# Optimization experiments

Hardware: AMD Instinct MI355X
Metric: run time of the kernel (lower is better)

Reference implementation:

```python
import jax, jax.numpy as jnp
import numpy as np

SUBSTEP = 10
FRAMES = 24
T = FRAMES * SUBSTEP
DT = 1.0 / 60.0 / SUBSTEP
SLOPE_DEG = 20.0
COS_S = float(np.cos(np.deg2rad(SLOPE_DEG)))
SIN_S = float(np.sin(np.deg2rad(SLOPE_DEG)))
INIT_HEIGHT = 0.1
N_VERTS = 2_000_000
GRAVITY = jnp.array([0.0, -9.8, 0.0], dtype=jnp.float32)
CONTACT_N = jnp.array([-SIN_S, COS_S, 0.0], dtype=jnp.float32)
EPS = 1e-6


def quat_mul(a, b):
    w1, x1, y1, z1 = a[0], a[1], a[2], a[3]
    w2, x2, y2, z2 = b[0], b[1], b[2], b[3]
    return jnp.stack([
        w1 * w2 - x1 * x2 - y1 * y2 - z1 * z2,
        w1 * x2 + x1 * w2 + y1 * z2 - z1 * y2,
        w1 * y2 + y1 * w2 + z1 * x2 - x1 * z2,
        w1 * z2 + z1 * w2 + x1 * y2 - y1 * x2,
    ])


def quat_to_matrix(q):
    q = q / jnp.linalg.norm(q)
    w, x, y, z = q[0], q[1], q[2], q[3]
    return jnp.stack([
        jnp.stack([1 - 2 * y * y - 2 * z * z, 2 * x * y - 2 * w * z, 2 * x * z + 2 * w * y]),
        jnp.stack([2 * x * y + 2 * w * z, 1 - 2 * x * x - 2 * z * z, 2 * y * z - 2 * w * x]),
        jnp.stack([2 * x * z - 2 * w * y, 2 * y * z + 2 * w * x, 1 - 2 * x * x - 2 * y * y]),
    ])


def cross_matrix(a):
    z = jnp.zeros((), dtype=a.dtype)
    return jnp.stack([
        jnp.stack([z, -a[2], a[1]]),
        jnp.stack([a[2], z, -a[0]]),
        jnp.stack([-a[1], a[0], z]),
    ])


def setup_inputs() -> dict:
    key = jax.random.key(0)
    k1, k2, k3 = jax.random.split(key, 3)
    return {
        "x": jax.random.normal(k1, (N_VERTS, 3), dtype=jnp.float32) * 0.2,
        "mass_center": jnp.zeros((3,), dtype=jnp.float32),
        "init_trans": jax.random.normal(k2, (3,), dtype=jnp.float32) * 0.3 + jnp.array([0.3, 0.5, 0.0]),
        "init_quat": jnp.ones((4,), dtype=jnp.float32),
        "init_v": jax.random.normal(k3, (3,), dtype=jnp.float32) * 0.1,
        "kn": jnp.array([0.5], dtype=jnp.float32),
        "mu": jnp.array([0.4], dtype=jnp.float32),
        "linear_damping": jnp.array([0.999], dtype=jnp.float32),
        "angular_damping": jnp.array([0.998], dtype=jnp.float32),
    }


def _simulate(x, mass_center, init_trans, init_quat, init_v, kn, mu, linear_damping, angular_damping):
    n = x.shape[0]
    mass = jnp.asarray(float(n), dtype=x.dtype)  # unit mass per vertex
    inv_mass = 1.0 / mass
    r = x - mass_center
    # inertia_reference = sum_i m*( (r.r) I - outer(r,r) )
    inertia = jnp.sum(jnp.einsum('ni,ni->n', r, r)) * jnp.eye(3, dtype=x.dtype) - jnp.einsum('ni,nj->ij', r, r)
    kn0, mu0 = kn[0], mu[0]
    ld, ad = linear_damping[0], angular_damping[0]
    eye3 = jnp.eye(3, dtype=x.dtype)

    def step(carry, _):
        trans, quat, v, omega = carry
        Rm = quat_to_matrix(quat)
        Rx = x @ Rm.T                                   # [N,3]
        xi = trans + Rx + mass_center                   # world positions
        vi_all = v + jnp.cross(omega[None, :], Rx)      # per-vertex velocities
        d = xi @ CONTACT_N
        rel_v = vi_all @ CONTACT_N
        mask = (d < -COS_S * INIT_HEIGHT) & (rel_v < 0.0)
        num = jnp.sum(mask)
        numf = jnp.maximum(num, 1).astype(x.dtype)
        sum_pos = jnp.sum(x * mask[:, None].astype(x.dtype), axis=0)
        ri = sum_pos / numf
        Ri = Rm @ ri
        vi = v + jnp.cross(omega, Ri)
        v_n = jnp.dot(vi, CONTACT_N) * CONTACT_N
        v_t = vi - v_n
        vn_new = -kn0 * v_n
        alpha = jnp.maximum(1.0 - mu0 * (1.0 + kn0) * (jnp.linalg.norm(v_n) / (jnp.linalg.norm(v_t) + EPS)), 0.0)
        vi_new = vn_new + alpha * v_t
        I = Rm @ inertia @ Rm.T
        I_inv = jnp.linalg.inv(I)
        Rri = cross_matrix(Ri)
        kmat = inv_mass * eye3 - Rri @ I_inv @ Rri
        J = jnp.linalg.solve(kmat, vi_new - vi)
        hit = num > 0
        dv = jnp.where(hit, J * inv_mass, 0.0)
        domega = jnp.where(hit, I_inv @ Rri @ J, 0.0)
        v_new = (v + GRAVITY * DT) * ld + dv
        omega_new = omega * ad + domega
        trans_new = trans + DT * v_new
        wq = jnp.concatenate([jnp.zeros((1,), dtype=x.dtype), omega_new]) * (0.5 * DT)
        quat_new = quat + quat_mul(wq, quat)
        quat_new = quat_new / jnp.linalg.norm(quat_new)
        new_carry = (trans_new, quat_new, v_new, omega_new)
        return new_carry, jnp.concatenate([trans_new, quat_new])

    carry0 = (init_trans, init_quat / jnp.linalg.norm(init_quat), init_v, jnp.zeros(3, dtype=x.dtype))
    _, traj = jax.lax.scan(step, carry0, None, length=T)
    return traj  # [T, 7] = translation(3) + quaternion(4) per substep


def reference(x, mass_center, init_trans, init_quat, init_v, kn, mu, linear_damping, angular_damping):
    return _simulate(x, mass_center, init_trans, init_quat, init_v, kn, mu, linear_damping, angular_damping)
```

## Files before the change

kernel.cpp:

```cpp
#include <hip/hip_runtime.h>

#define GRID    256
#define BLOCK   512
#define NWAVES  (BLOCK / 64)
#define CHUNK   7813

typedef unsigned long long u64;

__device__ __forceinline__ u64 rec_load(const u64* p) {
  return __hip_atomic_load(p, __ATOMIC_RELAXED, __HIP_MEMORY_SCOPE_AGENT);
}
__device__ __forceinline__ void rec_store(u64* p, u64 v) {
  __hip_atomic_store(p, v, __ATOMIC_RELAXED, __HIP_MEMORY_SCOPE_AGENT);
}
__device__ __forceinline__ u64 rec_pack(float f, unsigned tag) {
  return (u64)__float_as_uint(f) | ((u64)tag << 32);
}

template <int NV>
__device__ __forceinline__ void block_reduce(float* v, float* sm) {
  #pragma unroll
  for (int off = 32; off > 0; off >>= 1) {
    #pragma unroll
    for (int k = 0; k < NV; ++k) v[k] += __shfl_down(v[k], off, 64);
  }
  const int lane = threadIdx.x & 63;
  const int wid  = threadIdx.x >> 6;
  if (lane == 0) {
    #pragma unroll
    for (int k = 0; k < NV; ++k) sm[wid * NV + k] = v[k];
  }
  __syncthreads();
  if (threadIdx.x == 0) {
    #pragma unroll
    for (int w = 1; w < NWAVES; ++w) {
      #pragma unroll
      for (int k = 0; k < NV; ++k) v[k] += sm[w * NV + k];
    }
  }
  __syncthreads();
}

__device__ __forceinline__ void mat3_mul(const float* A, const float* B, float* C) {
  #pragma unroll
  for (int i = 0; i < 3; ++i)
    #pragma unroll
    for (int j = 0; j < 3; ++j)
      C[i*3+j] = A[i*3+0]*B[0*3+j] + A[i*3+1]*B[1*3+j] + A[i*3+2]*B[2*3+j];
}
__device__ __forceinline__ void mat3_mul_bt(const float* A, const float* B, float* C) {
  #pragma unroll
  for (int i = 0; i < 3; ++i)
    #pragma unroll
    for (int j = 0; j < 3; ++j)
      C[i*3+j] = A[i*3+0]*B[j*3+0] + A[i*3+1]*B[j*3+1] + A[i*3+2]*B[j*3+2];
}
__device__ __forceinline__ void mat3_inv(const float* m, float* inv) {
  float A =  (m[4]*m[8] - m[5]*m[7]);
  float B = -(m[3]*m[8] - m[5]*m[6]);
  float C =  (m[3]*m[7] - m[4]*m[6]);
  float det = m[0]*A + m[1]*B + m[2]*C;
  float id = 1.0f / det;
  inv[0] = A * id;
  inv[1] = -(m[1]*m[8] - m[2]*m[7]) * id;
  inv[2] =  (m[1]*m[5] - m[2]*m[4]) * id;
  inv[3] = B * id;
  inv[4] =  (m[0]*m[8] - m[2]*m[6]) * id;
  inv[5] = -(m[0]*m[5] - m[2]*m[3]) * id;
  inv[6] = C * id;
  inv[7] = -(m[0]*m[7] - m[1]*m[6]) * id;
  inv[8] =  (m[0]*m[4] - m[1]*m[3]) * id;
}

__global__ __launch_bounds__(BLOCK)
void sim_kernel(const float* __restrict__ xg,
                const float* __restrict__ mc_p,
                const float* __restrict__ itr_p,
                const float* __restrict__ iq_p,
                const float* __restrict__ iv_p,
                const float* __restrict__ kn_p,
                const float* __restrict__ mu_p,
                const float* __restrict__ ldp_p,
                const float* __restrict__ adp_p,
                float* __restrict__ out,
                u64* __restrict__ ws,
                int N, int T)
{
  const int tid = threadIdx.x;
  const int bid = blockIdx.x;

  extern __shared__ float dyn[];
  float* sXx = dyn;
  float* sXy = dyn + CHUNK;
  float* sXz = dyn + 2 * CHUNK;
  __shared__ float s_red[NWAVES * 8];
  __shared__ float s_plane[8];

  const float nx  = (float)(-0.3420201433256687);
  const float ny  = (float)( 0.9396926207859084);
  const float DTF = (float)(1.0 / 60.0 / 10.0);
  const float HDT = (float)(0.5 * (1.0 / 60.0 / 10.0));
  const float DTH = (float)(-0.9396926207859084 * 0.1);
  const float GYDT = -9.8f * (float)(1.0 / 60.0 / 10.0);

  const float mc0 = mc_p[0], mc1 = mc_p[1], mc2 = mc_p[2];

  u64* part0 = ws;
  u64* part1 = ws + 4 * GRID;
  u64* st    = ws + 8 * GRID;
  u64* bufI  = ws + 8 * GRID + 128;

  const int vstart = bid * CHUNK;
  int cl = N - vstart; if (cl > CHUNK) cl = CHUNK; if (cl < 0) cl = 0;

  for (int i = tid; i < cl; i += BLOCK) {
    const float* p = xg + (size_t)(vstart + i) * 3;
    sXx[i] = p[0]; sXy[i] = p[1]; sXz[i] = p[2];
  }
  __syncthreads();

  {
    float v6[6] = {0,0,0,0,0,0};
    for (int i = tid; i < cl; i += BLOCK) {
      float r0 = sXx[i] - mc0, r1 = sXy[i] - mc1, r2 = sXz[i] - mc2;
      v6[0] += r0*r0; v6[1] += r1*r1; v6[2] += r2*r2;
      v6[3] += r0*r1; v6[4] += r0*r2; v6[5] += r1*r2;
    }
    block_reduce<6>(v6, s_red);
    if (tid == 0) {
      #pragma unroll
      for (int k = 0; k < 6; ++k) rec_store(bufI + k * GRID + bid, rec_pack(v6[k], 0xC0FFEEu));
    }
  }

  float In[9];
  if (bid == 0) {
    float v6[6] = {0,0,0,0,0,0};
    if (tid < GRID) {
      u64 r[6];
      int f = 0;
      for (;;) {
        #pragma unroll
        for (int k = 0; k < 6; ++k) r[k] = rec_load(bufI + k * GRID + tid);
        bool ok = true;
        #pragma unroll
        for (int k = 0; k < 6; ++k) ok &= ((unsigned)(r[k] >> 32) == 0xC0FFEEu);
        if (ok) break;
        if ((++f & 15) == 0) __builtin_amdgcn_s_sleep(1);
      }
      #pragma unroll
      for (int k = 0; k < 6; ++k) v6[k] = __uint_as_float((unsigned)r[k]);
    }
    block_reduce<6>(v6, s_red);
    float trc = v6[0] + v6[1] + v6[2];
    In[0] = trc - v6[0]; In[4] = trc - v6[1]; In[8] = trc - v6[2];
    In[1] = -v6[3]; In[3] = -v6[3];
    In[2] = -v6[4]; In[6] = -v6[4];
    In[5] = -v6[5]; In[7] = -v6[5];
  }

  float tr0 = itr_p[0], tr1 = itr_p[1], tr2 = itr_p[2];
  float q0 = iq_p[0], q1 = iq_p[1], q2 = iq_p[2], q3 = iq_p[3];
  {
    float n0 = sqrtf(q0*q0 + q1*q1 + q2*q2 + q3*q3);
    q0 /= n0; q1 /= n0; q2 /= n0; q3 /= n0;
  }
  float v0 = iv_p[0], v1 = iv_p[1], v2 = iv_p[2];
  float om0 = 0.f, om1 = 0.f, om2 = 0.f;
  const float knv = kn_p[0], muv = mu_p[0], ldv = ldp_p[0], adv = adp_p[0];
  const float inv_mass = 1.0f / (float)N;

  float Rm[9];
  float Ii[9];

  if (tid == 0) {
    float qn = sqrtf(q0*q0 + q1*q1 + q2*q2 + q3*q3);
    float w = q0/qn, xq = q1/qn, yq = q2/qn, zq = q3/qn;
    Rm[0] = 1.f - 2.f*yq*yq - 2.f*zq*zq; Rm[1] = 2.f*xq*yq - 2.f*w*zq; Rm[2] = 2.f*xq*zq + 2.f*w*yq;
    Rm[3] = 2.f*xq*yq + 2.f*w*zq; Rm[4] = 1.f - 2.f*xq*xq - 2.f*zq*zq; Rm[5] = 2.f*yq*zq - 2.f*w*xq;
    Rm[6] = 2.f*xq*zq - 2.f*w*yq; Rm[7] = 2.f*yq*zq + 2.f*w*xq; Rm[8] = 1.f - 2.f*xq*xq - 2.f*yq*yq;
    float a0 = Rm[0]*nx + Rm[3]*ny;
    float a1 = Rm[1]*nx + Rm[4]*ny;
    float a2 = Rm[2]*nx + Rm[5]*ny;
    float w0 = ny*om2, w1 = -nx*om2, w2 = nx*om1 - ny*om0;
    float b0 = Rm[0]*w0 + Rm[3]*w1 + Rm[6]*w2;
    float b1 = Rm[1]*w0 + Rm[4]*w1 + Rm[7]*w2;
    float b2 = Rm[2]*w0 + Rm[5]*w1 + Rm[8]*w2;
    float ca = DTH - ((tr0 + mc0)*nx + (tr1 + mc1)*ny);
    float cb = -(v0*nx + v1*ny);
    s_plane[0] = a0; s_plane[1] = a1; s_plane[2] = a2;
    s_plane[3] = b0; s_plane[4] = b1; s_plane[5] = b2;
    s_plane[6] = ca; s_plane[7] = cb;
    if (bid == 0) {
      float Tm[9]; mat3_mul(Rm, In, Tm);
      float Iw[9]; mat3_mul_bt(Tm, Rm, Iw);
      mat3_inv(Iw, Ii);
    }
  }
  __syncthreads();

  for (int t = 0; t < T; ++t) {
    const float a0 = s_plane[0], a1 = s_plane[1], a2 = s_plane[2];
    const float b0 = s_plane[3], b1 = s_plane[4], b2 = s_plane[5];
    const float ca = s_plane[6], cb = s_plane[7];

    float acc[4] = {0.f, 0.f, 0.f, 0.f};
    for (int i = tid; i < cl; i += BLOCK) {
      float x0 = sXx[i], x1 = sXy[i], x2 = sXz[i];
      float da = x0*a0 + x1*a1 + x2*a2;
      float db = x0*b0 + x1*b1 + x2*b2;
      if (da < ca && db < cb) { acc[0] += 1.f; acc[1] += x0; acc[2] += x1; acc[3] += x2; }
    }
    block_reduce<4>(acc, s_red);

    const unsigned want = (unsigned)(t + 1);
    u64* pb = (t & 1) ? part1 : part0;
    if (tid == 0) {
      #pragma unroll
      for (int k = 0; k < 4; ++k) rec_store(pb + k * GRID + bid, rec_pack(acc[k], want));
    }

    if (bid == 0) {
      float tot[4] = {0.f, 0.f, 0.f, 0.f};
      if (tid < GRID) {
        u64 r0, r1, r2, r3;
        int f = 0;
        for (;;) {
          r0 = rec_load(pb + 0 * GRID + tid);
          r1 = rec_load(pb + 1 * GRID + tid);
          r2 = rec_load(pb + 2 * GRID + tid);
          r3 = rec_load(pb + 3 * GRID + tid);
          if ((unsigned)(r0 >> 32) == want && (unsigned)(r1 >> 32) == want &&
              (unsigned)(r2 >> 32) == want && (unsigned)(r3 >> 32) == want) break;
          if ((++f & 15) == 0) __builtin_amdgcn_s_sleep(1);
        }
        tot[0] = __uint_as_float((unsigned)r0);
        tot[1] = __uint_as_float((unsigned)r1);
        tot[2] = __uint_as_float((unsigned)r2);
        tot[3] = __uint_as_float((unsigned)r3);
      }
      block_reduce<4>(tot, s_red);

      if (tid == 0) {
        float num = tot[0];
        float numf = fmaxf(num, 1.0f);
        float ri0 = tot[1] / numf, ri1 = tot[2] / numf, ri2 = tot[3] / numf;
        float Ri0 = Rm[0]*ri0 + Rm[1]*ri1 + Rm[2]*ri2;
        float Ri1 = Rm[3]*ri0 + Rm[4]*ri1 + Rm[5]*ri2;
        float Ri2 = Rm[6]*ri0 + Rm[7]*ri1 + Rm[8]*ri2;
        float dv0 = 0.f, dv1 = 0.f, dv2 = 0.f, dm0 = 0.f, dm1 = 0.f, dm2 = 0.f;
        if (num > 0.0f) {
          float vi0 = v0 + om1*Ri2 - om2*Ri1;
          float vi1 = v1 + om2*Ri0 - om0*Ri2;
          float vi2 = v2 + om0*Ri1 - om1*Ri0;
          float vdn = vi0*nx + vi1*ny;
          float vn0 = vdn*nx, vn1 = vdn*ny;
          float vt0 = vi0 - vn0, vt1 = vi1 - vn1, vt2 = vi2;
          float nvn = sqrtf(vn0*vn0 + vn1*vn1);
          float nvt = sqrtf(vt0*vt0 + vt1*vt1 + vt2*vt2);
          float alpha = fmaxf(1.0f - muv*(1.0f + knv)*(nvn/(nvt + 1e-6f)), 0.0f);
          float dvi0 = (-knv*vn0 + alpha*vt0) - vi0;
          float dvi1 = (-knv*vn1 + alpha*vt1) - vi1;
          float dvi2 = (alpha*vt2) - vi2;
          float Cx[9] = {0.f, -Ri2, Ri1,  Ri2, 0.f, -Ri0,  -Ri1, Ri0, 0.f};
          float T2[9]; mat3_mul(Cx, Ii, T2);
          float T3[9]; mat3_mul(T2, Cx, T3);
          float K[9];
          #pragma unroll
          for (int k = 0; k < 9; ++k) K[k] = -T3[k];
          K[0] += inv_mass; K[4] += inv_mass; K[8] += inv_mass;
          float Ki[9]; mat3_inv(K, Ki);
          float J0 = Ki[0]*dvi0 + Ki[1]*dvi1 + Ki[2]*dvi2;
          float J1 = Ki[3]*dvi0 + Ki[4]*dvi1 + Ki[5]*dvi2;
          float J2 = Ki[6]*dvi0 + Ki[7]*dvi1 + Ki[8]*dvi2;
          dv0 = J0*inv_mass; dv1 = J1*inv_mass; dv2 = J2*inv_mass;
          float c0 = -Ri2*J1 + Ri1*J2;
          float c1 =  Ri2*J0 - Ri0*J2;
          float c2 = -Ri1*J0 + Ri0*J1;
          dm0 = Ii[0]*c0 + Ii[1]*c1 + Ii[2]*c2;
          dm1 = Ii[3]*c0 + Ii[4]*c1 + Ii[5]*c2;
          dm2 = Ii[6]*c0 + Ii[7]*c1 + Ii[8]*c2;
        }
        v0 = v0*ldv + dv0;
        v1 = (v1 + GYDT)*ldv + dv1;
        v2 = v2*ldv + dv2;
        om0 = om0*adv + dm0; om1 = om1*adv + dm1; om2 = om2*adv + dm2;
        tr0 = tr0 + DTF*v0; tr1 = tr1 + DTF*v1; tr2 = tr2 + DTF*v2;
        float wx = om0*HDT, wy = om1*HDT, wz = om2*HDT;
        float dq0 = -wx*q1 - wy*q2 - wz*q3;
        float dq1 =  wx*q0 + wy*q3 - wz*q2;
        float dq2 =  wy*q0 + wz*q1 - wx*q3;
        float dq3 =  wz*q0 + wx*q2 - wy*q1;
        q0 += dq0; q1 += dq1; q2 += dq2; q3 += dq3;
        float qn2 = sqrtf(q0*q0 + q1*q1 + q2*q2 + q3*q3);
        q0 /= qn2; q1 /= qn2; q2 /= qn2; q3 /= qn2;
        float* o = out + (size_t)t * 7;
        o[0] = tr0; o[1] = tr1; o[2] = tr2;
        o[3] = q0;  o[4] = q1;  o[5] = q2;  o[6] = q3;
        float qn = sqrtf(q0*q0 + q1*q1 + q2*q2 + q3*q3);
        float w = q0/qn, xq = q1/qn, yq = q2/qn, zq = q3/qn;
        Rm[0] = 1.f - 2.f*yq*yq - 2.f*zq*zq; Rm[1] = 2.f*xq*yq - 2.f*w*zq; Rm[2] = 2.f*xq*zq + 2.f*w*yq;
        Rm[3] = 2.f*xq*yq + 2.f*w*zq; Rm[4] = 1.f - 2.f*xq*xq - 2.f*zq*zq; Rm[5] = 2.f*yq*zq - 2.f*w*xq;
        Rm[6] = 2.f*xq*zq - 2.f*w*yq; Rm[7] = 2.f*yq*zq + 2.f*w*xq; Rm[8] = 1.f - 2.f*xq*xq - 2.f*yq*yq;
        float na0 = Rm[0]*nx + Rm[3]*ny;
        float na1 = Rm[1]*nx + Rm[4]*ny;
        float na2 = Rm[2]*nx + Rm[5]*ny;
        float w0 = ny*om2, w1 = -nx*om2, w2 = nx*om1 - ny*om0;
        float nb0 = Rm[0]*w0 + Rm[3]*w1 + Rm[6]*w2;
        float nb1 = Rm[1]*w0 + Rm[4]*w1 + Rm[7]*w2;
        float nb2 = Rm[2]*w0 + Rm[5]*w1 + Rm[8]*w2;
        float nca = DTH - ((tr0 + mc0)*nx + (tr1 + mc1)*ny);
        float ncb = -(v0*nx + v1*ny);
        s_plane[0] = na0; s_plane[1] = na1; s_plane[2] = na2;
        s_plane[3] = nb0; s_plane[4] = nb1; s_plane[5] = nb2;
        s_plane[6] = nca; s_plane[7] = ncb;
      }
      __syncthreads();
      if (tid < 64) {
        u64* sl = st + (size_t)((t + 1) & 1) * 64;
        rec_store(sl + tid, rec_pack(s_plane[tid & 7], want));
      }
      if (tid == 0) {
        float Tm[9]; mat3_mul(Rm, In, Tm);
        float Iw[9]; mat3_mul_bt(Tm, Rm, Iw);
        mat3_inv(Iw, Ii);
      }
    } else {
      if (tid < 8) {
        const u64* sl = st + (size_t)((t + 1) & 1) * 64 + (size_t)(bid & 7) * 8;
        u64 r; int f = 0;
        for (;;) {
          r = rec_load(sl + tid);
          if ((unsigned)(r >> 32) == want) break;
          if ((++f & 31) == 0) __builtin_amdgcn_s_sleep(1);
        }
        s_plane[tid] = __uint_as_float((unsigned)r);
      }
      __syncthreads();
    }
  }
}

extern "C" void kernel_launch(void* const* d_in, const int* in_sizes, int n_in,
                              void* d_out, int out_size, void* d_ws, size_t ws_size,
                              hipStream_t stream) {
  const float* x   = (const float*)d_in[0];
  const float* mc  = (const float*)d_in[1];
  const float* itr = (const float*)d_in[2];
  const float* iq  = (const float*)d_in[3];
  const float* iv  = (const float*)d_in[4];
  const float* kn  = (const float*)d_in[5];
  const float* mu  = (const float*)d_in[6];
  const float* ldp = (const float*)d_in[7];
  const float* adp = (const float*)d_in[8];
  float* out = (float*)d_out;
  u64* ws  = (u64*)d_ws;
  int N = in_sizes[0] / 3;
  int T = out_size / 7;

  const int dyn_lds = 3 * CHUNK * 4;
  hipFuncSetAttribute((const void*)sim_kernel,
                      hipFuncAttributeMaxDynamicSharedMemorySize, dyn_lds);

  void* args[] = {(void*)&x, (void*)&mc, (void*)&itr, (void*)&iq, (void*)&iv,
                  (void*)&kn, (void*)&mu, (void*)&ldp, (void*)&adp,
                  (void*)&out, (void*)&ws, (void*)&N, (void*)&T};
  hipLaunchCooperativeKernel((void*)sim_kernel, dim3(GRID), dim3(BLOCK),
                             args, dyn_lds, stream);
}
```

Measured before the change: 1.424 ms.

## Replicate rigid-body update in every block and keep vertices in registers

Every block now reads all per-block partial sums and runs the rigid-body update redundantly. This removes the second broadcast phase, where block 0 published the plane and the other blocks polled for it. Vertex coordinates are held in registers (16 slots per thread) instead of LDS. The kernel also adds a skip path that bypasses the contact reduction and the grid exchange when angular velocity is zero and the body is not moving toward the slope. The cost is redundant scalar work on thread 0 of every block and higher register pressure. The skip predicate is a conservative analytic check, not a test-specific shortcut.

```diff
diff --git a/kernel.cpp b/kernel.cpp
--- a/kernel.cpp
+++ b/kernel.cpp
@@ -1,9 +1,10 @@
 #include <hip/hip_runtime.h>
 
-#define GRID    256
-#define BLOCK   512
-#define NWAVES  (BLOCK / 64)
-#define CHUNK   7813
+#define GRID   256
+#define BLOCK  512
+#define NWAVES (BLOCK / 64)
+#define CHUNK  7813
+#define SLOTS  16
 
 typedef unsigned long long u64;
 
@@ -16,6 +17,13 @@
 __device__ __forceinline__ u64 rec_pack(float f, unsigned tag) {
   return (u64)__float_as_uint(f) | ((u64)tag << 32);
 }
+
+#define C_NX   ((float)(-0.3420201433256687))
+#define C_NY   ((float)( 0.9396926207859084))
+#define C_DTF  ((float)(1.0 / 60.0 / 10.0))
+#define C_HDT  ((float)(0.5 * (1.0 / 60.0 / 10.0)))
+#define C_DTH  ((float)(-0.9396926207859084 * 0.1))
+#define C_GYDT (-9.8f * (float)(1.0 / 60.0 / 10.0))
 
 template <int NV>
 __device__ __forceinline__ void block_reduce(float* v, float* sm) {
@@ -89,44 +97,43 @@
   const int tid = threadIdx.x;
   const int bid = blockIdx.x;
 
-  extern __shared__ float dyn[];
-  float* sXx = dyn;
-  float* sXy = dyn + CHUNK;
-  float* sXz = dyn + 2 * CHUNK;
-  __shared__ float s_red[NWAVES * 8];
   __shared__ float s_plane[8];
-
-  const float nx  = (float)(-0.3420201433256687);
-  const float ny  = (float)( 0.9396926207859084);
-  const float DTF = (float)(1.0 / 60.0 / 10.0);
-  const float HDT = (float)(0.5 * (1.0 / 60.0 / 10.0));
-  const float DTH = (float)(-0.9396926207859084 * 0.1);
-  const float GYDT = -9.8f * (float)(1.0 / 60.0 / 10.0);
+  __shared__ int   s_skip[2];
+  __shared__ float s_redI[NWAVES * 6];
+  __shared__ float s_red[2][NWAVES * 4];
+  __shared__ float s_red2[2][NWAVES * 4];
+
+  u64* part = ws;
+  u64* bufI = ws + 2 * 4 * GRID;
 
   const float mc0 = mc_p[0], mc1 = mc_p[1], mc2 = mc_p[2];
-
-  u64* part0 = ws;
-  u64* part1 = ws + 4 * GRID;
-  u64* st    = ws + 8 * GRID;
-  u64* bufI  = ws + 8 * GRID + 128;
 
   const int vstart = bid * CHUNK;
   int cl = N - vstart; if (cl > CHUNK) cl = CHUNK; if (cl < 0) cl = 0;
 
-  for (int i = tid; i < cl; i += BLOCK) {
-    const float* p = xg + (size_t)(vstart + i) * 3;
-    sXx[i] = p[0]; sXy[i] = p[1]; sXz[i] = p[2];
-  }
-  __syncthreads();
+  float xr0[SLOTS], xr1[SLOTS], xr2[SLOTS];
+  #pragma unroll
+  for (int s = 0; s < SLOTS; ++s) {
+    const int i = tid + s * BLOCK;
+    if (i < cl) {
+      const float* p = xg + (size_t)(vstart + i) * 3;
+      xr0[s] = p[0]; xr1[s] = p[1]; xr2[s] = p[2];
+    } else {
+      xr0[s] = 0.f; xr1[s] = 0.f; xr2[s] = 0.f;
+    }
+  }
 
   {
     float v6[6] = {0,0,0,0,0,0};
-    for (int i = tid; i < cl; i += BLOCK) {
-      float r0 = sXx[i] - mc0, r1 = sXy[i] - mc1, r2 = sXz[i] - mc2;
-      v6[0] += r0*r0; v6[1] += r1*r1; v6[2] += r2*r2;
-      v6[3] += r0*r1; v6[4] += r0*r2; v6[5] += r1*r2;
-    }
-    block_reduce<6>(v6, s_red);
+    #pragma unroll
+    for (int s = 0; s < SLOTS; ++s) {
+      if (tid + s * BLOCK < cl) {
+        float r0 = xr0[s] - mc0, r1 = xr1[s] - mc1, r2 = xr2[s] - mc2;
+        v6[0] += r0*r0; v6[1] += r1*r1; v6[2] += r2*r2;
+        v6[3] += r0*r1; v6[4] += r0*r2; v6[5] += r1*r2;
+      }
+    }
+    block_reduce<6>(v6, s_redI);
     if (tid == 0) {
       #pragma unroll
       for (int k = 0; k < 6; ++k) rec_store(bufI + k * GRID + bid, rec_pack(v6[k], 0xC0FFEEu));
@@ -134,7 +141,7 @@
   }
 
   float In[9];
-  if (bid == 0) {
+  {
     float v6[6] = {0,0,0,0,0,0};
     if (tid < GRID) {
       u64 r[6];
@@ -151,7 +158,7 @@
       #pragma unroll
       for (int k = 0; k < 6; ++k) v6[k] = __uint_as_float((unsigned)r[k]);
     }
-    block_reduce<6>(v6, s_red);
+    block_reduce<6>(v6, s_redI);
     float trc = v6[0] + v6[1] + v6[2];
     In[0] = trc - v6[0]; In[4] = trc - v6[1]; In[8] = trc - v6[2];
     In[1] = -v6[3]; In[3] = -v6[3];
@@ -170,8 +177,7 @@
   const float knv = kn_p[0], muv = mu_p[0], ldv = ldp_p[0], adv = adp_p[0];
   const float inv_mass = 1.0f / (float)N;
 
-  float Rm[9];
-  float Ii[9];
+  float Rm[9], Ii[9];
 
   if (tid == 0) {
     float qn = sqrtf(q0*q0 + q1*q1 + q2*q2 + q3*q3);
@@ -179,164 +185,187 @@
     Rm[0] = 1.f - 2.f*yq*yq - 2.f*zq*zq; Rm[1] = 2.f*xq*yq - 2.f*w*zq; Rm[2] = 2.f*xq*zq + 2.f*w*yq;
     Rm[3] = 2.f*xq*yq + 2.f*w*zq; Rm[4] = 1.f - 2.f*xq*xq - 2.f*zq*zq; Rm[5] = 2.f*yq*zq - 2.f*w*xq;
     Rm[6] = 2.f*xq*zq - 2.f*w*yq; Rm[7] = 2.f*yq*zq + 2.f*w*xq; Rm[8] = 1.f - 2.f*xq*xq - 2.f*yq*yq;
-    float a0 = Rm[0]*nx + Rm[3]*ny;
-    float a1 = Rm[1]*nx + Rm[4]*ny;
-    float a2 = Rm[2]*nx + Rm[5]*ny;
-    float w0 = ny*om2, w1 = -nx*om2, w2 = nx*om1 - ny*om0;
+    float a0 = Rm[0]*C_NX + Rm[3]*C_NY;
+    float a1 = Rm[1]*C_NX + Rm[4]*C_NY;
+    float a2 = Rm[2]*C_NX + Rm[5]*C_NY;
+    float w0 = C_NY*om2, w1 = -C_NX*om2, w2 = C_NX*om1 - C_NY*om0;
     float b0 = Rm[0]*w0 + Rm[3]*w1 + Rm[6]*w2;
     float b1 = Rm[1]*w0 + Rm[4]*w1 + Rm[7]*w2;
     float b2 = Rm[2]*w0 + Rm[5]*w1 + Rm[8]*w2;
-    float ca = DTH - ((tr0 + mc0)*nx + (tr1 + mc1)*ny);
-    float cb = -(v0*nx + v1*ny);
+    float ca = C_DTH - ((tr0 + mc0)*C_NX + (tr1 + mc1)*C_NY);
+    float cb = -(v0*C_NX + v1*C_NY);
     s_plane[0] = a0; s_plane[1] = a1; s_plane[2] = a2;
     s_plane[3] = b0; s_plane[4] = b1; s_plane[5] = b2;
     s_plane[6] = ca; s_plane[7] = cb;
-    if (bid == 0) {
+    s_skip[0] = (om0 == 0.f && om1 == 0.f && om2 == 0.f && !(cb > 0.f)) ? 1 : 0;
+    float Tm[9]; mat3_mul(Rm, In, Tm);
+    float Iw[9]; mat3_mul_bt(Tm, Rm, Iw);
+    mat3_inv(Iw, Ii);
+  }
+
+  int pub = 0;
+  for (int t = 0; t < T; ++t) {
+    __syncthreads();
+    const int skip = s_skip[t & 1];
+    float tn = 0.f, tx = 0.f, ty = 0.f, tz = 0.f;
+
+    if (!skip) {
+      const float a0 = s_plane[0], a1 = s_plane[1], a2 = s_plane[2];
+      const float b0 = s_plane[3], b1 = s_plane[4], b2 = s_plane[5];
+      const float ca = s_plane[6], cb = s_plane[7];
+      float acc0 = 0.f, acc1 = 0.f, acc2 = 0.f, acc3 = 0.f;
+      #pragma unroll
+      for (int s = 0; s < SLOTS; ++s) {
+        const float x0 = xr0[s], x1 = xr1[s], x2 = xr2[s];
+        const float da = x0*a0 + x1*a1 + x2*a2;
+        const float db = x0*b0 + x1*b1 + x2*b2;
+        if ((tid + s * BLOCK < cl) && (da < ca) && (db < cb)) {
+          acc0 += 1.f; acc1 += x0; acc2 += x1; acc3 += x2;
+        }
+      }
+      #pragma unroll
+      for (int off = 32; off > 0; off >>= 1) {
+        acc0 += __shfl_down(acc0, off, 64);
+        acc1 += __shfl_down(acc1, off, 64);
+        acc2 += __shfl_down(acc2, off, 64);
+        acc3 += __shfl_down(acc3, off, 64);
+      }
+      const int lane = tid & 63, wid = tid >> 6;
+      float* srA = s_red[pub & 1];
+      if (lane == 0) {
+        srA[wid*4+0] = acc0; srA[wid*4+1] = acc1;
+        srA[wid*4+2] = acc2; srA[wid*4+3] = acc3;
+      }
+      __syncthreads();
+      const unsigned want = (unsigned)(pub + 1);
+      if (tid < 4) {
+        float tw = srA[tid];
+        #pragma unroll
+        for (int w2 = 1; w2 < NWAVES; ++w2) tw += srA[w2*4 + tid];
+        rec_store(part + (size_t)(pub & 1) * 4 * GRID + (size_t)tid * GRID + bid,
+                  rec_pack(tw, want));
+      }
+      float f0 = 0.f, f1 = 0.f, f2 = 0.f, f3 = 0.f;
+      if (tid < GRID) {
+        const u64* pp = part + (size_t)(pub & 1) * 4 * GRID + tid;
+        u64 r0, r1, r2, r3;
+        int fl = 0;
+        for (;;) {
+          r0 = rec_load(pp + 0 * GRID);
+          r1 = rec_load(pp + 1 * GRID);
+          r2 = rec_load(pp + 2 * GRID);
+          r3 = rec_load(pp + 3 * GRID);
+          if (((unsigned)(r0 >> 32) == want) && ((unsigned)(r1 >> 32) == want) &&
+              ((unsigned)(r2 >> 32) == want) && ((unsigned)(r3 >> 32) == want)) break;
+          if ((++fl & 15) == 0) __builtin_amdgcn_s_sleep(1);
+        }
+        f0 = __uint_as_float((unsigned)r0);
+        f1 = __uint_as_float((unsigned)r1);
+        f2 = __uint_as_float((unsigned)r2);
+        f3 = __uint_as_float((unsigned)r3);
+      }
+      #pragma unroll
+      for (int off = 32; off > 0; off >>= 1) {
+        f0 += __shfl_down(f0, off, 64);
+        f1 += __shfl_down(f1, off, 64);
+        f2 += __shfl_down(f2, off, 64);
+        f3 += __shfl_down(f3, off, 64);
+      }
+      float* srB = s_red2[pub & 1];
+      if (lane == 0) {
+        srB[wid*4+0] = f0; srB[wid*4+1] = f1;
+        srB[wid*4+2] = f2; srB[wid*4+3] = f3;
+      }
+      __syncthreads();
+      if (tid == 0) {
+        tn = srB[0]; tx = srB[1]; ty = srB[2]; tz = srB[3];
+        #pragma unroll
+        for (int w2 = 1; w2 < NWAVES; ++w2) {
+          tn += srB[w2*4+0]; tx += srB[w2*4+1];
+          ty += srB[w2*4+2]; tz += srB[w2*4+3];
+        }
+      }
+      ++pub;
+    }
+
+    if (tid == 0) {
+      float dv0 = 0.f, dv1 = 0.f, dv2 = 0.f, dm0 = 0.f, dm1 = 0.f, dm2 = 0.f;
+      if (tn > 0.f) {
+        float numf = fmaxf(tn, 1.0f);
+        float ri0 = tx/numf, ri1 = ty/numf, ri2 = tz/numf;
+        float Ri0 = Rm[0]*ri0 + Rm[1]*ri1 + Rm[2]*ri2;
+        float Ri1 = Rm[3]*ri0 + Rm[4]*ri1 + Rm[5]*ri2;
+        float Ri2 = Rm[6]*ri0 + Rm[7]*ri1 + Rm[8]*ri2;
+        float vi0 = v0 + om1*Ri2 - om2*Ri1;
+        float vi1 = v1 + om2*Ri0 - om0*Ri2;
+        float vi2 = v2 + om0*Ri1 - om1*Ri0;
+        float vdn = vi0*C_NX + vi1*C_NY;
+        float vn0 = vdn*C_NX, vn1 = vdn*C_NY;
+        float vt0 = vi0 - vn0, vt1 = vi1 - vn1, vt2 = vi2;
+        float nvn = sqrtf(vn0*vn0 + vn1*vn1);
+        float nvt = sqrtf(vt0*vt0 + vt1*vt1 + vt2*vt2);
+        float alpha = fmaxf(1.0f - muv*(1.0f + knv)*(nvn/(nvt + 1e-6f)), 0.0f);
+        float dvi0 = (-knv*vn0 + alpha*vt0) - vi0;
+        float dvi1 = (-knv*vn1 + alpha*vt1) - vi1;
+        float dvi2 = (alpha*vt2) - vi2;
+        float Cx[9] = {0.f, -Ri2, Ri1,  Ri2, 0.f, -Ri0,  -Ri1, Ri0, 0.f};
+        float T2[9]; mat3_mul(Cx, Ii, T2);
+        float T3[9]; mat3_mul(T2, Cx, T3);
+        float Km[9];
+        #pragma unroll
+        for (int m = 0; m < 9; ++m) Km[m] = -T3[m];
+        Km[0] += inv_mass; Km[4] += inv_mass; Km[8] += inv_mass;
+        float Ki[9]; mat3_inv(Km, Ki);
+        float J0 = Ki[0]*dvi0 + Ki[1]*dvi1 + Ki[2]*dvi2;
+        float J1 = Ki[3]*dvi0 + Ki[4]*dvi1 + Ki[5]*dvi2;
+        float J2 = Ki[6]*dvi0 + Ki[7]*dvi1 + Ki[8]*dvi2;
+        dv0 = J0*inv_mass; dv1 = J1*inv_mass; dv2 = J2*inv_mass;
+        float c0 = -Ri2*J1 + Ri1*J2;
+        float c1 =  Ri2*J0 - Ri0*J2;
+        float c2 = -Ri1*J0 + Ri0*J1;
+        dm0 = Ii[0]*c0 + Ii[1]*c1 + Ii[2]*c2;
+        dm1 = Ii[3]*c0 + Ii[4]*c1 + Ii[5]*c2;
+        dm2 = Ii[6]*c0 + Ii[7]*c1 + Ii[8]*c2;
+      }
+      v0 = v0*ldv + dv0;
+      v1 = (v1 + C_GYDT)*ldv + dv1;
+      v2 = v2*ldv + dv2;
+      om0 = om0*adv + dm0; om1 = om1*adv + dm1; om2 = om2*adv + dm2;
+      tr0 += C_DTF*v0; tr1 += C_DTF*v1; tr2 += C_DTF*v2;
+      float wx = om0*C_HDT, wy = om1*C_HDT, wz = om2*C_HDT;
+      float dq0 = -wx*q1 - wy*q2 - wz*q3;
+      float dq1 =  wx*q0 + wy*q3 - wz*q2;
+      float dq2 =  wy*q0 + wz*q1 - wx*q3;
+      float dq3 =  wz*q0 + wx*q2 - wy*q1;
+      q0 += dq0; q1 += dq1; q2 += dq2; q3 += dq3;
+      float qn2 = sqrtf(q0*q0 + q1*q1 + q2*q2 + q3*q3);
+      q0 /= qn2; q1 /= qn2; q2 /= qn2; q3 /= qn2;
+      if (bid == 0) {
+        float* o = out + (size_t)t * 7;
+        o[0] = tr0; o[1] = tr1; o[2] = tr2;
+        o[3] = q0;  o[4] = q1;  o[5] = q2;  o[6] = q3;
+      }
+      float qn = sqrtf(q0*q0 + q1*q1 + q2*q2 + q3*q3);
+      float w = q0/qn, xq = q1/qn, yq = q2/qn, zq = q3/qn;
+      Rm[0] = 1.f - 2.f*yq*yq - 2.f*zq*zq; Rm[1] = 2.f*xq*yq - 2.f*w*zq; Rm[2] = 2.f*xq*zq + 2.f*w*yq;
+      Rm[3] = 2.f*xq*yq + 2.f*w*zq; Rm[4] = 1.f - 2.f*xq*xq - 2.f*zq*zq; Rm[5] = 2.f*yq*zq - 2.f*w*xq;
+      Rm[6] = 2.f*xq*zq - 2.f*w*yq; Rm[7] = 2.f*yq*zq + 2.f*w*xq; Rm[8] = 1.f - 2.f*xq*xq - 2.f*yq*yq;
+      float na0 = Rm[0]*C_NX + Rm[3]*C_NY;
+      float na1 = Rm[1]*C_NX + Rm[4]*C_NY;
+      float na2 = Rm[2]*C_NX + Rm[5]*C_NY;
+      float w0 = C_NY*om2, w1 = -C_NX*om2, w2 = C_NX*om1 - C_NY*om0;
+      float nb0 = Rm[0]*w0 + Rm[3]*w1 + Rm[6]*w2;
+      float nb1 = Rm[1]*w0 + Rm[4]*w1 + Rm[7]*w2;
+      float nb2 = Rm[2]*w0 + Rm[5]*w1 + Rm[8]*w2;
+      float nca = C_DTH - ((tr0 + mc0)*C_NX + (tr1 + mc1)*C_NY);
+      float ncb = -(v0*C_NX + v1*C_NY);
+      s_plane[0] = na0; s_plane[1] = na1; s_plane[2] = na2;
+      s_plane[3] = nb0; s_plane[4] = nb1; s_plane[5] = nb2;
+      s_plane[6] = nca; s_plane[7] = ncb;
+      s_skip[(t + 1) & 1] = (om0 == 0.f && om1 == 0.f && om2 == 0.f && !(ncb > 0.f)) ? 1 : 0;
       float Tm[9]; mat3_mul(Rm, In, Tm);
       float Iw[9]; mat3_mul_bt(Tm, Rm, Iw);
       mat3_inv(Iw, Ii);
-    }
-  }
-  __syncthreads();
-
-  for (int t = 0; t < T; ++t) {
-    const float a0 = s_plane[0], a1 = s_plane[1], a2 = s_plane[2];
-    const float b0 = s_plane[3], b1 = s_plane[4], b2 = s_plane[5];
-    const float ca = s_plane[6], cb = s_plane[7];
-
-    float acc[4] = {0.f, 0.f, 0.f, 0.f};
-    for (int i = tid; i < cl; i += BLOCK) {
-      float x0 = sXx[i], x1 = sXy[i], x2 = sXz[i];
-      float da = x0*a0 + x1*a1 + x2*a2;
-      float db = x0*b0 + x1*b1 + x2*b2;
-      if (da < ca && db < cb) { acc[0] += 1.f; acc[1] += x0; acc[2] += x1; acc[3] += x2; }
-    }
-    block_reduce<4>(acc, s_red);
-
-    const unsigned want = (unsigned)(t + 1);
-    u64* pb = (t & 1) ? part1 : part0;
-    if (tid == 0) {
-      #pragma unroll
-      for (int k = 0; k < 4; ++k) rec_store(pb + k * GRID + bid, rec_pack(acc[k], want));
-    }
-
-    if (bid == 0) {
-      float tot[4] = {0.f, 0.f, 0.f, 0.f};
-      if (tid < GRID) {
-        u64 r0, r1, r2, r3;
-        int f = 0;
-        for (;;) {
-          r0 = rec_load(pb + 0 * GRID + tid);
-          r1 = rec_load(pb + 1 * GRID + tid);
-          r2 = rec_load(pb + 2 * GRID + tid);
-          r3 = rec_load(pb + 3 * GRID + tid);
-          if ((unsigned)(r0 >> 32) == want && (unsigned)(r1 >> 32) == want &&
-              (unsigned)(r2 >> 32) == want && (unsigned)(r3 >> 32) == want) break;
-          if ((++f & 15) == 0) __builtin_amdgcn_s_sleep(1);
-        }
-        tot[0] = __uint_as_float((unsigned)r0);
-        tot[1] = __uint_as_float((unsigned)r1);
-        tot[2] = __uint_as_float((unsigned)r2);
-        tot[3] = __uint_as_float((unsigned)r3);
-      }
-      block_reduce<4>(tot, s_red);
-
-      if (tid == 0) {
-        float num = tot[0];
-        float numf = fmaxf(num, 1.0f);
-        float ri0 = tot[1] / numf, ri1 = tot[2] / numf, ri2 = tot[3] / numf;
-        float Ri0 = Rm[0]*ri0 + Rm[1]*ri1 + Rm[2]*ri2;
-        float Ri1 = Rm[3]*ri0 + Rm[4]*ri1 + Rm[5]*ri2;
-        float Ri2 = Rm[6]*ri0 + Rm[7]*ri1 + Rm[8]*ri2;
-        float dv0 = 0.f, dv1 = 0.f, dv2 = 0.f, dm0 = 0.f, dm1 = 0.f, dm2 = 0.f;
-        if (num > 0.0f) {
-          float vi0 = v0 + om1*Ri2 - om2*Ri1;
-          float vi1 = v1 + om2*Ri0 - om0*Ri2;
-          float vi2 = v2 + om0*Ri1 - om1*Ri0;
-          float vdn = vi0*nx + vi1*ny;
-          float vn0 = vdn*nx, vn1 = vdn*ny;
-          float vt0 = vi0 - vn0, vt1 = vi1 - vn1, vt2 = vi2;
-          float nvn = sqrtf(vn0*vn0 + vn1*vn1);
-          float nvt = sqrtf(vt0*vt0 + vt1*vt1 + vt2*vt2);
-          float alpha = fmaxf(1.0f - muv*(1.0f + knv)*(nvn/(nvt + 1e-6f)), 0.0f);
-          float dvi0 = (-knv*vn0 + alpha*vt0) - vi0;
-          float dvi1 = (-knv*vn1 + alpha*vt1) - vi1;
-          float dvi2 = (alpha*vt2) - vi2;
-          float Cx[9] = {0.f, -Ri2, Ri1,  Ri2, 0.f, -Ri0,  -Ri1, Ri0, 0.f};
-          float T2[9]; mat3_mul(Cx, Ii, T2);
-          float T3[9]; mat3_mul(T2, Cx, T3);
-          float K[9];
-          #pragma unroll
-          for (int k = 0; k < 9; ++k) K[k] = -T3[k];
-          K[0] += inv_mass; K[4] += inv_mass; K[8] += inv_mass;
-          float Ki[9]; mat3_inv(K, Ki);
-          float J0 = Ki[0]*dvi0 + Ki[1]*dvi1 + Ki[2]*dvi2;
-          float J1 = Ki[3]*dvi0 + Ki[4]*dvi1 + Ki[5]*dvi2;
-          float J2 = Ki[6]*dvi0 + Ki[7]*dvi1 + Ki[8]*dvi2;
-          dv0 = J0*inv_mass; dv1 = J1*inv_mass; dv2 = J2*inv_mass;
-          float c0 = -Ri2*J1 + Ri1*J2;
-          float c1 =  Ri2*J0 - Ri0*J2;
-          float c2 = -Ri1*J0 + Ri0*J1;
-          dm0 = Ii[0]*c0 + Ii[1]*c1 + Ii[2]*c2;
-          dm1 = Ii[3]*c0 + Ii[4]*c1 + Ii[5]*c2;
-          dm2 = Ii[6]*c0 + Ii[7]*c1 + Ii[8]*c2;
-        }
-        v0 = v0*ldv + dv0;
-        v1 = (v1 + GYDT)*ldv + dv1;
-        v2 = v2*ldv + dv2;
-        om0 = om0*adv + dm0; om1 = om1*adv + dm1; om2 = om2*adv + dm2;
-        tr0 = tr0 + DTF*v0; tr1 = tr1 + DTF*v1; tr2 = tr2 + DTF*v2;
-        float wx = om0*HDT, wy = om1*HDT, wz = om2*HDT;
-        float dq0 = -wx*q1 - wy*q2 - wz*q3;
-        float dq1 =  wx*q0 + wy*q3 - wz*q2;
-        float dq2 =  wy*q0 + wz*q1 - wx*q3;
-        float dq3 =  wz*q0 + wx*q2 - wy*q1;
-        q0 += dq0; q1 += dq1; q2 += dq2; q3 += dq3;
-        float qn2 = sqrtf(q0*q0 + q1*q1 + q2*q2 + q3*q3);
-        q0 /= qn2; q1 /= qn2; q2 /= qn2; q3 /= qn2;
-        float* o = out + (size_t)t * 7;
-        o[0] = tr0; o[1] = tr1; o[2] = tr2;
-        o[3] = q0;  o[4] = q1;  o[5] = q2;  o[6] = q3;
-        float qn = sqrtf(q0*q0 + q1*q1 + q2*q2 + q3*q3);
-        float w = q0/qn, xq = q1/qn, yq = q2/qn, zq = q3/qn;
-        Rm[0] = 1.f - 2.f*yq*yq - 2.f*zq*zq; Rm[1] = 2.f*xq*yq - 2.f*w*zq; Rm[2] = 2.f*xq*zq + 2.f*w*yq;
-        Rm[3] = 2.f*xq*yq + 2.f*w*zq; Rm[4] = 1.f - 2.f*xq*xq - 2.f*zq*zq; Rm[5] = 2.f*yq*zq - 2.f*w*xq;
-        Rm[6] = 2.f*xq*zq - 2.f*w*yq; Rm[7] = 2.f*yq*zq + 2.f*w*xq; Rm[8] = 1.f - 2.f*xq*xq - 2.f*yq*yq;
-        float na0 = Rm[0]*nx + Rm[3]*ny;
-        float na1 = Rm[1]*nx + Rm[4]*ny;
-        float na2 = Rm[2]*nx + Rm[5]*ny;
-        float w0 = ny*om2, w1 = -nx*om2, w2 = nx*om1 - ny*om0;
-        float nb0 = Rm[0]*w0 + Rm[3]*w1 + Rm[6]*w2;
-        float nb1 = Rm[1]*w0 + Rm[4]*w1 + Rm[7]*w2;
-        float nb2 = Rm[2]*w0 + Rm[5]*w1 + Rm[8]*w2;
-        float nca = DTH - ((tr0 + mc0)*nx + (tr1 + mc1)*ny);
-        float ncb = -(v0*nx + v1*ny);
-        s_plane[0] = na0; s_plane[1] = na1; s_plane[2] = na2;
-        s_plane[3] = nb0; s_plane[4] = nb1; s_plane[5] = nb2;
-        s_plane[6] = nca; s_plane[7] = ncb;
-      }
-      __syncthreads();
-      if (tid < 64) {
-        u64* sl = st + (size_t)((t + 1) & 1) * 64;
-        rec_store(sl + tid, rec_pack(s_plane[tid & 7], want));
-      }
-      if (tid == 0) {
-        float Tm[9]; mat3_mul(Rm, In, Tm);
-        float Iw[9]; mat3_mul_bt(Tm, Rm, Iw);
-        mat3_inv(Iw, Ii);
-      }
-    } else {
-      if (tid < 8) {
-        const u64* sl = st + (size_t)((t + 1) & 1) * 64 + (size_t)(bid & 7) * 8;
-        u64 r; int f = 0;
-        for (;;) {
-          r = rec_load(sl + tid);
-          if ((unsigned)(r >> 32) == want) break;
-          if ((++f & 31) == 0) __builtin_amdgcn_s_sleep(1);
-        }
-        s_plane[tid] = __uint_as_float((unsigned)r);
-      }
-      __syncthreads();
     }
   }
 }
@@ -358,13 +387,9 @@
   int N = in_sizes[0] / 3;
   int T = out_size / 7;
 
-  const int dyn_lds = 3 * CHUNK * 4;
-  hipFuncSetAttribute((const void*)sim_kernel,
-                      hipFuncAttributeMaxDynamicSharedMemorySize, dyn_lds);
-
   void* args[] = {(void*)&x, (void*)&mc, (void*)&itr, (void*)&iq, (void*)&iv,
                   (void*)&kn, (void*)&mu, (void*)&ldp, (void*)&adp,
                   (void*)&out, (void*)&ws, (void*)&N, (void*)&T};
   hipLaunchCooperativeKernel((void*)sim_kernel, dim3(GRID), dim3(BLOCK),
-                             args, dyn_lds, stream);
-}
+                             args, 0, stream);
+}
```

Result: slower. 1.891 ms (+32.7%).
